# Optimization experiments

Hardware: AMD Instinct MI355X
Metric: run time of the kernel (lower is better)

The kernel has to match this reference:

```python
import jax, jax.numpy as jnp
import numpy as np

K_PRED = 6
SCORE_TEMP = 0.5
MPA_THRESH = (2.5, 1.0, 2.0)   # meters, [veh, ped, cyc]
MTR_THRESH = (2.5, 1.0, 2.0)
TRACK_FUTURE = 91 - 11          # step_gt - step_current = 80


def setup_inputs() -> dict:
    key = jax.random.key(0)
    k1, k2, k3 = jax.random.split(key, 3)
    n_sc, n_ag, n_jf, n_step = 64, 64, 32, 80
    # scale 2.0 so endpoint pair distances straddle the ~2.5m NMS thresholds
    trajs = jax.random.normal(k1, (n_sc, n_jf, n_ag, n_step, 3), dtype=jnp.float32) * 2.0
    scores = jax.random.normal(k2, (n_sc, n_jf, n_ag), dtype=jnp.float32)
    ag_idx = jax.random.randint(k3, (n_sc, n_ag), 0, 3)
    ag_type = jax.nn.one_hot(ag_idx, 3, dtype=jnp.float32)  # [n_sc, n_ag, 3] one-hot
    return {"ag_type": ag_type, "trajs": trajs, "scores": scores}


def _type_thresh(ag_type, thresh_list):
    # ag_type [S,A,3] one-hot -> per-agent threshold [S,A]
    return ag_type @ jnp.asarray(thresh_list, dtype=ag_type.dtype)


def _endpoint_within(trajs, thresh):
    # use_ade=False: pairwise distance of final-step xy. trajs [S,A,J,T,3]
    end_xy = trajs[:, :, :, -1, :2]  # [S,A,J,2]
    d = jnp.linalg.norm(end_xy[:, :, :, None, :] - end_xy[:, :, None, :, :], axis=-1)
    return d < thresh[:, :, None, None]  # [S,A,J,J] bool


def _mtr_nms(trajs, scores, within, k_pred):
    # greedy: pick argmax, down-weight nearby modes by 0.01, kill picked with -1
    def step(sc, _):
        idx = jnp.argmax(sc, axis=-1)  # [S,A]
        w = jnp.take_along_axis(within, idx[:, :, None, None], axis=2)[:, :, 0]  # [S,A,J]
        sc = sc * ((~w).astype(sc.dtype) * 0.99 + 0.01)
        sc = jnp.where(jax.nn.one_hot(idx, sc.shape[-1], dtype=bool), -1.0, sc)
        return sc, idx

    _, idxs = jax.lax.scan(step, scores, None, length=k_pred)
    mode_idx = jnp.moveaxis(idxs, 0, -1)  # [S,A,k_pred]
    trajs_k = jnp.take_along_axis(trajs, mode_idx[:, :, :, None, None], axis=2)
    scores_k = jnp.take_along_axis(scores, mode_idx, axis=2)
    return trajs_k, scores_k / scores_k.sum(-1, keepdims=True)


def _mpa_nms_agent(scores, within):
    # scores [K], within [K,K]; visit modes in descending original-score order,
    # suppress mode k to 0.001 if any currently-higher-scoring mode is within thresh.
    order = jnp.argsort(-scores)

    def step(sc, k):
        mask = within[k] & (sc > sc[k])
        return sc.at[k].set(jnp.where(mask.any(), 0.001, sc[k])), None

    sc, _ = jax.lax.scan(step, scores, order)
    return sc


def reference(ag_type, trajs, scores):
    trajs = jnp.swapaxes(trajs, 1, 2)  # [S,A,J,T,3]
    scores = jax.nn.softmax(jnp.swapaxes(scores, 1, 2), axis=-1)  # [S,A,J]

    # mtr_nms: reduce n_joint_future -> k_pred (mtr_nms_thresh non-empty, aggr empty)
    within = _endpoint_within(trajs, _type_thresh(ag_type, MTR_THRESH))
    trajs, scores = _mtr_nms(trajs, scores, within, K_PRED)

    # mpa_nms: rescore the k_pred modes
    within = _endpoint_within(trajs, _type_thresh(ag_type, MPA_THRESH))
    scores = jax.vmap(jax.vmap(_mpa_nms_agent))(scores, within)
    scores = scores / scores.sum(-1, keepdims=True)

    # score temperature > 0
    scores = jax.nn.softmax(jnp.log(scores) / SCORE_TEMP, axis=-1)

    # downsample to 2Hz: [S,A,k_pred,16,3]
    return trajs[:, :, :, 4:TRACK_FUTURE:5], scores
```

## Files before the change

### kernel.cpp

```cpp
#include <hip/hip_runtime.h>


#define NSC 64
#define NAG 64
#define NJF 32
#define NSTEP 80
#define KP 6
#define TOUT 16

struct F3 { float x, y, z; };

__global__ __launch_bounds__(64)
void womd_pp10(const float* __restrict__ ag_type,
               const float* __restrict__ trajs,
               const float* __restrict__ scores,
               float* __restrict__ out)
{
    const int tid = threadIdx.x;
    const int g   = tid >> 4;
    const int gl  = tid & 15;
    const int ga  = blockIdx.x * 4 + g;
    const int s   = ga >> 6;
    const int a   = ga & 63;

    const float* sp = scores + (size_t)s * NJF * NAG + a;
    float raw0 = sp[(size_t)gl * NAG];
    float raw1 = sp[(size_t)(gl + 16) * NAG];

    const float* tb = trajs + (size_t)s * NJF * NAG * NSTEP * 3;
    size_t e0 = (((size_t)gl * NAG + a) * NSTEP + (NSTEP - 1)) * 3;
    size_t e1 = (((size_t)(gl + 16) * NAG + a) * NSTEP + (NSTEP - 1)) * 3;
    float2 p0 = *(const float2*)(tb + e0);
    float2 p1 = *(const float2*)(tb + e1);

    F3 atv = *(const F3*)(ag_type + (size_t)(s * NAG + a) * 3);
    const float thresh = atv.x * 2.5f + atv.y * 1.0f + atv.z * 2.0f;

    float mx = fmaxf(raw0, raw1);
    #pragma unroll
    for (int off = 8; off > 0; off >>= 1)
        mx = fmaxf(mx, __shfl_xor(mx, off, 16));
    float ev0 = expf(raw0 - mx);
    float ev1 = expf(raw1 - mx);
    float sum = ev0 + ev1;
    #pragma unroll
    for (int off = 8; off > 0; off >>= 1)
        sum += __shfl_xor(sum, off, 16);
    float sm0 = ev0 / sum;
    float sm1 = ev1 / sum;

    int   sel[KP];
    float skp[KP], sxp[KP], syp[KP];
    float ls0 = sm0, ls1 = sm1;
    #pragma unroll
    for (int k = 0; k < KP; ++k) {
        float v = fmaxf(ls0, ls1);
        #pragma unroll
        for (int off = 8; off > 0; off >>= 1)
            v = fmaxf(v, __shfl_xor(v, off, 16));
        unsigned long long b0 = __ballot(ls0 == v);
        unsigned long long b1 = __ballot(ls1 == v);
        unsigned m0 = (unsigned)(b0 >> (g * 16)) & 0xFFFFu;
        unsigned m1 = (unsigned)(b1 >> (g * 16)) & 0xFFFFu;
        int idx = m0 ? (__ffs(m0) - 1) : (16 + __ffs(m1) - 1);
        sel[k] = idx;

        int  il = idx & 15;
        bool lo = (idx < 16);
        float sxv = lo ? p0.x : p1.x;
        float syv = lo ? p0.y : p1.y;
        float skv = lo ? sm0 : sm1;
        float px = __shfl(sxv, il, 16);
        float py = __shfl(syv, il, 16);
        float pk = __shfl(skv, il, 16);
        sxp[k] = px;  syp[k] = py;  skp[k] = pk;

        float dx0 = p0.x - px, dy0 = p0.y - py;
        float dx1 = p1.x - px, dy1 = p1.y - py;
        bool w0 = sqrtf(dx0 * dx0 + dy0 * dy0) < thresh;
        bool w1 = sqrtf(dx1 * dx1 + dy1 * dy1) < thresh;
        ls0 *= w0 ? 0.01f : 1.0f;
        ls1 *= w1 ? 0.01f : 1.0f;
        ls0 = (gl == idx)      ? -1.0f : ls0;
        ls1 = (gl + 16 == idx) ? -1.0f : ls1;
    }

    F3 pt[KP];
    #pragma unroll
    for (int i = 0; i < KP; ++i) {
        size_t src = (((size_t)sel[i] * NAG + a) * NSTEP + (4 + 5 * gl)) * 3;
        pt[i] = *(const F3*)(tb + src);
    }

    float ssum = 0.f;
    #pragma unroll
    for (int k = 0; k < KP; ++k) ssum += skp[k];
    float sk[KP], sk0[KP];
    #pragma unroll
    for (int k = 0; k < KP; ++k) { sk[k] = skp[k] / ssum; sk0[k] = sk[k]; }

    unsigned w2[KP];
    #pragma unroll
    for (int i = 0; i < KP; ++i) {
        unsigned r = 0;
        #pragma unroll
        for (int j = 0; j < KP; ++j) {
            float dx = sxp[i] - sxp[j], dy = syp[i] - syp[j];
            r |= (sqrtf(dx * dx + dy * dy) < thresh) ? (1u << j) : 0u;
        }
        w2[i] = r;
    }

    int rank[KP];
    #pragma unroll
    for (int j = 0; j < KP; ++j) {
        int r = 0;
        #pragma unroll
        for (int i = 0; i < KP; ++i)
            r += ((sk0[i] > sk0[j]) || (sk0[i] == sk0[j] && i < j)) ? 1 : 0;
        rank[j] = r;
    }

    #pragma unroll
    for (int t = 0; t < KP; ++t) {
        float sk_k = sk[0]; unsigned w2k = w2[0];
        #pragma unroll
        for (int j = 1; j < KP; ++j) {
            bool is = (rank[j] == t);
            sk_k = is ? sk[j] : sk_k;
            w2k  = is ? w2[j] : w2k;
        }
        bool any = false;
        #pragma unroll
        for (int j = 0; j < KP; ++j)
            any = any || ((((w2k >> j) & 1u) != 0u) && (sk[j] > sk_k));
        #pragma unroll
        for (int j = 0; j < KP; ++j)
            if (rank[j] == t && any) sk[j] = 0.001f;
    }

    float s2 = 0.f;
    #pragma unroll
    for (int k = 0; k < KP; ++k) s2 += sk[k];
    #pragma unroll
    for (int k = 0; k < KP; ++k) sk[k] /= s2;
    float q[KP]; float s3 = 0.f;
    #pragma unroll
    for (int k = 0; k < KP; ++k) { q[k] = sk[k] * sk[k]; s3 += q[k]; }

    float qs = q[0] / s3;
    qs = (gl == 1) ? q[1] / s3 : qs;
    qs = (gl == 2) ? q[2] / s3 : qs;
    qs = (gl == 3) ? q[3] / s3 : qs;
    qs = (gl == 4) ? q[4] / s3 : qs;
    qs = (gl == 5) ? q[5] / s3 : qs;
    const size_t SCBASE = (size_t)NSC * NAG * KP * TOUT * 3;
    if (gl < KP) out[SCBASE + (size_t)ga * KP + gl] = qs;

    size_t ob = (size_t)ga * (KP * TOUT * 3);
    #pragma unroll
    for (int i = 0; i < KP; ++i)
        *(F3*)(out + ob + (size_t)(16 * i + gl) * 3) = pt[i];
}

extern "C" void kernel_launch(void* const* d_in, const int* in_sizes, int n_in,
                              void* d_out, int out_size, void* d_ws, size_t ws_size,
                              hipStream_t stream) {
    const float* ag_type = (const float*)d_in[0];
    const float* trajs   = (const float*)d_in[1];
    const float* scores  = (const float*)d_in[2];
    float* out = (float*)d_out;

    womd_pp10<<<NSC * NAG / 4, 64, 0, stream>>>(ag_type, trajs, scores, out);
}
```

Before: 28.35 us.

## Pack eight agents per wavefront with four modes per lane

Each group of 16 lanes per agent shrinks to 8 lanes, so one 64-thread block now serves 8 agents and the grid is half as large. Each lane holds four modes and gathers two output timesteps. The argmax now does a shuffle reduction carrying (value, index) with lowest-index tie-breaking in place of the ballot/ffs lookup, giving shorter reductions and fewer blocks in exchange for more per-lane work and fewer lanes issuing the scattered gathers.

```diff
diff --git a/kernel.cpp b/kernel.cpp
--- a/kernel.cpp
+++ b/kernel.cpp
@@ -11,85 +11,94 @@
 struct F3 { float x, y, z; };
 
 __global__ __launch_bounds__(64)
-void womd_pp10(const float* __restrict__ ag_type,
+void womd_pp11(const float* __restrict__ ag_type,
                const float* __restrict__ trajs,
                const float* __restrict__ scores,
                float* __restrict__ out)
 {
     const int tid = threadIdx.x;
-    const int g   = tid >> 4;
-    const int gl  = tid & 15;
-    const int ga  = blockIdx.x * 4 + g;
+    const int g   = tid >> 3;
+    const int o   = tid & 7;
+    const int ga  = blockIdx.x * 8 + g;
     const int s   = ga >> 6;
     const int a   = ga & 63;
 
     const float* sp = scores + (size_t)s * NJF * NAG + a;
-    float raw0 = sp[(size_t)gl * NAG];
-    float raw1 = sp[(size_t)(gl + 16) * NAG];
+    float raw0 = sp[(size_t)(o)      * NAG];
+    float raw1 = sp[(size_t)(o + 8)  * NAG];
+    float raw2 = sp[(size_t)(o + 16) * NAG];
+    float raw3 = sp[(size_t)(o + 24) * NAG];
 
     const float* tb = trajs + (size_t)s * NJF * NAG * NSTEP * 3;
-    size_t e0 = (((size_t)gl * NAG + a) * NSTEP + (NSTEP - 1)) * 3;
-    size_t e1 = (((size_t)(gl + 16) * NAG + a) * NSTEP + (NSTEP - 1)) * 3;
-    float2 p0 = *(const float2*)(tb + e0);
-    float2 p1 = *(const float2*)(tb + e1);
+    #define EOFF(j) ((((size_t)(j) * NAG + a) * NSTEP + (NSTEP - 1)) * 3)
+    float2 p0 = *(const float2*)(tb + EOFF(o));
+    float2 p1 = *(const float2*)(tb + EOFF(o + 8));
+    float2 p2 = *(const float2*)(tb + EOFF(o + 16));
+    float2 p3 = *(const float2*)(tb + EOFF(o + 24));
 
     F3 atv = *(const F3*)(ag_type + (size_t)(s * NAG + a) * 3);
     const float thresh = atv.x * 2.5f + atv.y * 1.0f + atv.z * 2.0f;
 
-    float mx = fmaxf(raw0, raw1);
+    float mx = fmaxf(fmaxf(raw0, raw1), fmaxf(raw2, raw3));
     #pragma unroll
-    for (int off = 8; off > 0; off >>= 1)
-        mx = fmaxf(mx, __shfl_xor(mx, off, 16));
+    for (int off = 4; off > 0; off >>= 1)
+        mx = fmaxf(mx, __shfl_xor(mx, off, 8));
     float ev0 = expf(raw0 - mx);
     float ev1 = expf(raw1 - mx);
-    float sum = ev0 + ev1;
+    float ev2 = expf(raw2 - mx);
+    float ev3 = expf(raw3 - mx);
+    float sum = ev0 + ev1 + ev2 + ev3;
     #pragma unroll
-    for (int off = 8; off > 0; off >>= 1)
-        sum += __shfl_xor(sum, off, 16);
-    float sm0 = ev0 / sum;
-    float sm1 = ev1 / sum;
+    for (int off = 4; off > 0; off >>= 1)
+        sum += __shfl_xor(sum, off, 8);
+    float sm0 = ev0 / sum, sm1 = ev1 / sum, sm2 = ev2 / sum, sm3 = ev3 / sum;
 
     int   sel[KP];
     float skp[KP], sxp[KP], syp[KP];
-    float ls0 = sm0, ls1 = sm1;
+    float ls0 = sm0, ls1 = sm1, ls2 = sm2, ls3 = sm3;
     #pragma unroll
     for (int k = 0; k < KP; ++k) {
-        float v = fmaxf(ls0, ls1);
+        float v = ls0; int idx = o;
+        if (ls1 > v) { v = ls1; idx = o + 8; }
+        if (ls2 > v) { v = ls2; idx = o + 16; }
+        if (ls3 > v) { v = ls3; idx = o + 24; }
         #pragma unroll
-        for (int off = 8; off > 0; off >>= 1)
-            v = fmaxf(v, __shfl_xor(v, off, 16));
-        unsigned long long b0 = __ballot(ls0 == v);
-        unsigned long long b1 = __ballot(ls1 == v);
-        unsigned m0 = (unsigned)(b0 >> (g * 16)) & 0xFFFFu;
-        unsigned m1 = (unsigned)(b1 >> (g * 16)) & 0xFFFFu;
-        int idx = m0 ? (__ffs(m0) - 1) : (16 + __ffs(m1) - 1);
+        for (int off = 4; off > 0; off >>= 1) {
+            float ov = __shfl_xor(v, off, 8);
+            int   oi = __shfl_xor(idx, off, 8);
+            if (ov > v || (ov == v && oi < idx)) { v = ov; idx = oi; }
+        }
         sel[k] = idx;
 
-        int  il = idx & 15;
-        bool lo = (idx < 16);
-        float sxv = lo ? p0.x : p1.x;
-        float syv = lo ? p0.y : p1.y;
-        float skv = lo ? sm0 : sm1;
-        float px = __shfl(sxv, il, 16);
-        float py = __shfl(syv, il, 16);
-        float pk = __shfl(skv, il, 16);
+        int reg = idx >> 3;
+        float sxv = (reg == 0) ? p0.x : (reg == 1) ? p1.x : (reg == 2) ? p2.x : p3.x;
+        float syv = (reg == 0) ? p0.y : (reg == 1) ? p1.y : (reg == 2) ? p2.y : p3.y;
+        float skv = (reg == 0) ? sm0  : (reg == 1) ? sm1  : (reg == 2) ? sm2  : sm3;
+        float px = __shfl(sxv, idx & 7, 8);
+        float py = __shfl(syv, idx & 7, 8);
+        float pk = __shfl(skv, idx & 7, 8);
         sxp[k] = px;  syp[k] = py;  skp[k] = pk;
 
         float dx0 = p0.x - px, dy0 = p0.y - py;
         float dx1 = p1.x - px, dy1 = p1.y - py;
-        bool w0 = sqrtf(dx0 * dx0 + dy0 * dy0) < thresh;
-        bool w1 = sqrtf(dx1 * dx1 + dy1 * dy1) < thresh;
-        ls0 *= w0 ? 0.01f : 1.0f;
-        ls1 *= w1 ? 0.01f : 1.0f;
-        ls0 = (gl == idx)      ? -1.0f : ls0;
-        ls1 = (gl + 16 == idx) ? -1.0f : ls1;
+        float dx2 = p2.x - px, dy2 = p2.y - py;
+        float dx3 = p3.x - px, dy3 = p3.y - py;
+        ls0 *= (sqrtf(dx0 * dx0 + dy0 * dy0) < thresh) ? 0.01f : 1.0f;
+        ls1 *= (sqrtf(dx1 * dx1 + dy1 * dy1) < thresh) ? 0.01f : 1.0f;
+        ls2 *= (sqrtf(dx2 * dx2 + dy2 * dy2) < thresh) ? 0.01f : 1.0f;
+        ls3 *= (sqrtf(dx3 * dx3 + dy3 * dy3) < thresh) ? 0.01f : 1.0f;
+        ls0 = (idx == o)      ? -1.0f : ls0;
+        ls1 = (idx == o + 8)  ? -1.0f : ls1;
+        ls2 = (idx == o + 16) ? -1.0f : ls2;
+        ls3 = (idx == o + 24) ? -1.0f : ls3;
     }
 
-    F3 pt[KP];
+    F3 ptA[KP], ptB[KP];
     #pragma unroll
-    for (int i = 0; i < KP; ++i) {
-        size_t src = (((size_t)sel[i] * NAG + a) * NSTEP + (4 + 5 * gl)) * 3;
-        pt[i] = *(const F3*)(tb + src);
+    for (int m = 0; m < KP; ++m) {
+        size_t row = ((size_t)sel[m] * NAG + a) * NSTEP;
+        ptA[m] = *(const F3*)(tb + (row + (4 + 5 * o)) * 3);
+        ptB[m] = *(const F3*)(tb + (row + (4 + 5 * (o + 8))) * 3);
     }
 
     float ssum = 0.f;
@@ -149,18 +158,20 @@
     for (int k = 0; k < KP; ++k) { q[k] = sk[k] * sk[k]; s3 += q[k]; }
 
     float qs = q[0] / s3;
-    qs = (gl == 1) ? q[1] / s3 : qs;
-    qs = (gl == 2) ? q[2] / s3 : qs;
-    qs = (gl == 3) ? q[3] / s3 : qs;
-    qs = (gl == 4) ? q[4] / s3 : qs;
-    qs = (gl == 5) ? q[5] / s3 : qs;
+    qs = (o == 1) ? q[1] / s3 : qs;
+    qs = (o == 2) ? q[2] / s3 : qs;
+    qs = (o == 3) ? q[3] / s3 : qs;
+    qs = (o == 4) ? q[4] / s3 : qs;
+    qs = (o == 5) ? q[5] / s3 : qs;
     const size_t SCBASE = (size_t)NSC * NAG * KP * TOUT * 3;
-    if (gl < KP) out[SCBASE + (size_t)ga * KP + gl] = qs;
+    if (o < KP) out[SCBASE + (size_t)ga * KP + o] = qs;
 
     size_t ob = (size_t)ga * (KP * TOUT * 3);
     #pragma unroll
-    for (int i = 0; i < KP; ++i)
-        *(F3*)(out + ob + (size_t)(16 * i + gl) * 3) = pt[i];
+    for (int m = 0; m < KP; ++m) {
+        *(F3*)(out + ob + (size_t)(16 * m + o) * 3)     = ptA[m];
+        *(F3*)(out + ob + (size_t)(16 * m + o + 8) * 3) = ptB[m];
+    }
 }
 
 extern "C" void kernel_launch(void* const* d_in, const int* in_sizes, int n_in,
@@ -171,5 +182,5 @@
     const float* scores  = (const float*)d_in[2];
     float* out = (float*)d_out;
 
-    womd_pp10<<<NSC * NAG / 4, 64, 0, stream>>>(ag_type, trajs, scores, out);
+    womd_pp11<<<NSC * NAG / 8, 64, 0, stream>>>(ag_type, trajs, scores, out);
 }
```

New measurement: 42.49 us. +49.9%, slower.
